# Performance work log

Hardware: AMD Instinct MI355X
Metric: run time of the kernel (lower is better)

The kernel has to match this reference:

```python
import jax, jax.numpy as jnp
import numpy as np

NUM_LAYERS = 3


def setup_inputs() -> dict:
    key = jax.random.key(0)
    k1, k2, k3 = jax.random.split(key, 3)
    B, LT, LC, F = 16, 256, 768, 256
    batch_target = jax.random.normal(k1, (B, LT, F), dtype=jnp.float32)
    batch_claim = jax.random.normal(k2, (B, LC, F), dtype=jnp.float32)
    # adjacency is accepted but mathematically unused (original masked_fill is non-in-place and discarded)
    batch_adj = jax.random.randint(jax.random.fold_in(key, 7), (B, LT + LC, LT + LC), 0, 2, dtype=jnp.int32)
    # per-layer trans_linear weights, nn.Linear(F, F, bias=False): y = x @ W.T, W is [out, in]
    W_trans = jax.random.normal(k3, (NUM_LAYERS, F, F), dtype=jnp.float32) * (1.0 / np.sqrt(F))
    return {"batch_target": batch_target, "batch_claim": batch_claim, "batch_adj": batch_adj, "W_trans": W_trans}


def _gcn_layer(node_rep, W):
    # dot attention: score[b,i,j] = <h_i, h_j>  (symmetric all-pairs dot product)
    # NOTE: original's masked_fill(batch_adj == 0, -1e9) is NOT in-place and its
    # result is discarded, so no masking is applied -- reproduced faithfully here.
    corr = jnp.einsum('bif,bjf->bij', node_rep, node_rep)
    attn = jax.nn.softmax(corr, axis=2)              # softmax over j (dim=2)
    trans = jnp.einsum('blf,gf->blg', node_rep, W)   # trans_linear (bias=False)
    node_out = jax.nn.relu(node_rep + jnp.einsum('bij,bjf->bif', attn, trans))
    return node_out, attn


def reference(batch_target, batch_claim, batch_adj, W_trans):
    target_len = batch_target.shape[1]
    node_rep = jnp.concatenate([batch_target, batch_claim], axis=1)  # [B, L, F]
    all_node_rep, all_corr_score = (), ()
    for i in range(NUM_LAYERS):
        node_rep, corr_score = _gcn_layer(node_rep, W_trans[i])
        all_node_rep = all_node_rep + (node_rep,)
        all_corr_score = all_corr_score + (corr_score,)
        # gcn_dropout: identity in eval mode
    target_rep = node_rep[:, :target_len, :]
    claim_rep = node_rep[:, target_len:, :]
    return (target_rep, claim_rep, all_node_rep, all_corr_score)
```

## Files before the change

### kernel.cpp

```cpp
#include <hip/hip_runtime.h>

typedef _Float16 h16;
typedef _Float16 h16x8 __attribute__((ext_vector_type(8)));
typedef _Float16 h16x4 __attribute__((ext_vector_type(4)));
typedef float    f32x4 __attribute__((ext_vector_type(4)));
typedef float    f32x8 __attribute__((ext_vector_type(8)));

#define NBATCH 16
#define LROWS  1024
#define FDIM   256

#define OFF_TGT 0ull
#define OFF_CLM 1048576ull
#define OFF_NR  4194304ull
#define OFF_AT  16777216ull

__device__ __forceinline__ void split2(float x, h16& h, h16& l) {
    h = (h16)x;
    l = (h16)(x - (float)h);
}

typedef const __attribute__((address_space(1))) void gvoid;
typedef __attribute__((address_space(3))) void lvoid;
__device__ __forceinline__ void gl_lds16(const void* g, void* l) {
    __builtin_amdgcn_global_load_lds((gvoid*)g, (lvoid*)l, 16, 0, 0);
}

__device__ const unsigned char TRI_I[36] = {
    0,0,0,0,0,0,0,0, 1,1,1,1,1,1,1, 2,2,2,2,2,2, 3,3,3,3,3, 4,4,4,4, 5,5,5, 6,6, 7};
__device__ const unsigned char TRI_J[36] = {
    0,1,2,3,4,5,6,7, 1,2,3,4,5,6,7, 2,3,4,5,6,7, 3,4,5,6,7, 4,5,6,7, 5,6,7, 6,7, 7};

__global__ __launch_bounds__(256) void convert_all(const float* __restrict__ tgt,
                                                   const float* __restrict__ clm,
                                                   const float* __restrict__ W,
                                                   h16* __restrict__ xh, h16* __restrict__ xl,
                                                   h16* __restrict__ wh) {
    int bid = blockIdx.x;
    if (bid < 4096) {
        int b, i;
        if (bid < 2048) { b = bid & 7;       i = bid >> 3; }
        else            { b = 8 + (bid & 7); i = (bid - 2048) >> 3; }
        size_t e = ((size_t)b << 18) + (size_t)i * 1024 + (size_t)threadIdx.x * 4;
        int rf = (int)(e & 262143);
        int r  = rf >> 8, f = rf & 255;
        const float* src = (r < 256)
            ? tgt + ((size_t)b << 16) + ((size_t)r << 8) + f
            : clm + (size_t)b * 196608 + ((size_t)(r - 256) << 8) + f;
        f32x4 v = *(const f32x4*)src;
        h16x4 hv, lv;
#pragma unroll
        for (int j = 0; j < 4; ++j) { h16 hh, ll; split2(v[j], hh, ll); hv[j] = hh; lv[j] = ll; }
        *(h16x4*)(xh + e) = hv;
        *(h16x4*)(xl + e) = lv;
    } else {
        size_t e = ((size_t)(bid - 4096) * 256 + threadIdx.x) * 4;
        f32x4 v = *(const f32x4*)(W + e);
        h16x4 hv;
#pragma unroll
        for (int j = 0; j < 4; ++j) hv[j] = (h16)v[j];
        *(h16x4*)(wh + e) = hv;
    }
}

__global__ __launch_bounds__(256, 3) void gemm_ct(
    const h16* __restrict__ Xh, const h16* __restrict__ Xl,
    const h16* __restrict__ Wh,
    h16* __restrict__ Ptil, float2* __restrict__ part,
    h16* __restrict__ Th) {
    int b, u;
    if (blockIdx.x < 416) { b = blockIdx.x & 7;               u = blockIdx.x >> 3; }
    else                  { b = 8 + ((blockIdx.x - 416) & 7); u = (blockIdx.x - 416) >> 3; }
    const bool isCorr = u < 36;
    int it, jt;
    if (isCorr) { it = TRI_I[u]; jt = TRI_J[u]; }
    else        { int v = u - 36; it = v >> 1; jt = v & 1; }
    const bool diag = isCorr && (it == jt);
    const int i0 = it * 128;
    const int j0 = jt * 128;
    const int t  = threadIdx.x;
    const int lane = t & 63, wid = t >> 6;
    const int wr = wid >> 1, wc = wid & 1;

    __shared__ alignas(16) char lds[32768];

    const size_t arow = ((size_t)b * LROWS + i0) * 256;
    const h16* bHp; const h16* bLp; size_t brow;
    if (isCorr) { bHp = Xh; bLp = Xl; brow = ((size_t)b * LROWS + j0) * 256; }
    else        { bHp = Wh; bLp = Xl; brow = (size_t)j0 * 256; }

    const int bOffH = diag ? 0 : 16384;
    const int bOffL = diag ? 8192 : 24576;

    f32x4 acc[4][4];
#pragma unroll
    for (int i = 0; i < 4; ++i)
#pragma unroll
        for (int j = 0; j < 4; ++j) acc[i][j] = (f32x4){0.f, 0.f, 0.f, 0.f};

    const int grow = t >> 2;
    const int gq   = t & 3;

    for (int kt = 0; kt < 8; ++kt) {
        __syncthreads();
#pragma unroll
        for (int p = 0; p < 2; ++p) {
            int r = p * 64 + grow;
            size_t so = (size_t)r * 256 + kt * 32 + ((gq ^ ((r >> 1) & 3)) << 3);
            char* d = lds + p * 4096 + wid * 1024;
            gl_lds16(Xh + arow + so, d);
            gl_lds16(Xl + arow + so, d + 8192);
            if (!diag) {
                gl_lds16(bHp + brow + so, d + 16384);
                if (isCorr) gl_lds16(bLp + brow + so, d + 24576);
            }
        }
        __syncthreads();

        const int kq = lane >> 4;
        const int rA = wr * 64 + (lane & 15);
        const int rB = wc * 64 + (lane & 15);
        h16x8 ah[4], al[4], bh[4], bl[4];
#pragma unroll
        for (int mi = 0; mi < 4; ++mi) {
            int r   = rA + mi * 16;
            int off = r * 64 + ((kq ^ ((r >> 1) & 3)) << 4);
            ah[mi] = *(const h16x8*)(lds + off);
            al[mi] = *(const h16x8*)(lds + 8192 + off);
        }
#pragma unroll
        for (int nj = 0; nj < 4; ++nj) {
            int r   = rB + nj * 16;
            int off = r * 64 + ((kq ^ ((r >> 1) & 3)) << 4);
            bh[nj] = *(const h16x8*)(lds + bOffH + off);
            if (isCorr) bl[nj] = *(const h16x8*)(lds + bOffL + off);
        }
        __builtin_amdgcn_s_setprio(1);
#pragma unroll
        for (int mi = 0; mi < 4; ++mi)
#pragma unroll
            for (int nj = 0; nj < 4; ++nj) {
                acc[mi][nj] = __builtin_amdgcn_mfma_f32_16x16x32_f16(ah[mi], bh[nj], acc[mi][nj], 0, 0, 0);
                acc[mi][nj] = __builtin_amdgcn_mfma_f32_16x16x32_f16(al[mi], bh[nj], acc[mi][nj], 0, 0, 0);
                if (isCorr)
                    acc[mi][nj] = __builtin_amdgcn_mfma_f32_16x16x32_f16(ah[mi], bl[nj], acc[mi][nj], 0, 0, 0);
            }
        __builtin_amdgcn_s_setprio(0);
    }

    const int mBase = i0 + wr * 64;
    const int nBase = j0 + wc * 64;
    if (isCorr) {
        h16* Pb = Ptil + (size_t)b * LROWS * 1024;
        {
            const int chunk = jt * 2 + wc;
#pragma unroll
            for (int mi = 0; mi < 4; ++mi)
#pragma unroll
                for (int rg = 0; rg < 4; ++rg) {
                    float v0 = acc[mi][0][rg], v1 = acc[mi][1][rg];
                    float v2 = acc[mi][2][rg], v3 = acc[mi][3][rg];
                    float mx = fmaxf(fmaxf(v0, v1), fmaxf(v2, v3));
#pragma unroll
                    for (int off = 8; off >= 1; off >>= 1) mx = fmaxf(mx, __shfl_xor(mx, off, 64));
                    float e0 = __expf(v0 - mx), e1 = __expf(v1 - mx);
                    float e2 = __expf(v2 - mx), e3 = __expf(v3 - mx);
                    float s = e0 + e1 + e2 + e3;
#pragma unroll
                    for (int off = 8; off >= 1; off >>= 1) s += __shfl_xor(s, off, 64);
                    int row = mBase + mi * 16 + ((lane >> 4) * 4) + rg;
                    if ((lane & 15) == 0)
                        part[((size_t)b * 1024 + row) * 16 + chunk] = make_float2(mx, s);
                    size_t rb = (size_t)row * 1024 + nBase + (lane & 15);
                    Pb[rb]      = (h16)e0;
                    Pb[rb + 16] = (h16)e1;
                    Pb[rb + 32] = (h16)e2;
                    Pb[rb + 48] = (h16)e3;
                }
        }
        if (it != jt) {
            __syncthreads();
            const int chunk = it * 2 + wr;
            const int cl0 = wc * 64 + (lane & 15);
            const int r40 = wr * 64 + ((lane >> 4) << 2);
#pragma unroll
            for (int nj = 0; nj < 4; ++nj) {
                float mx = -3.0e38f;
#pragma unroll
                for (int mi = 0; mi < 4; ++mi)
#pragma unroll
                    for (int rg = 0; rg < 4; ++rg) mx = fmaxf(mx, acc[mi][nj][rg]);
                mx = fmaxf(mx, __shfl_xor(mx, 16, 64));
                mx = fmaxf(mx, __shfl_xor(mx, 32, 64));
                float s = 0.f;
                h16x4 pt[4];
#pragma unroll
                for (int mi = 0; mi < 4; ++mi)
#pragma unroll
                    for (int rg = 0; rg < 4; ++rg) {
                        float e = __expf(acc[mi][nj][rg] - mx);
                        s += e;
                        pt[mi][rg] = (h16)e;
                    }
                s += __shfl_xor(s, 16, 64);
                s += __shfl_xor(s, 32, 64);
                int n = nBase + nj * 16 + (lane & 15);
                if (lane < 16)
                    part[((size_t)b * 1024 + n) * 16 + chunk] = make_float2(mx, s);
                const int cl = cl0 + nj * 16;
#pragma unroll
                for (int mi = 0; mi < 4; ++mi) {
                    int r4 = r40 + mi * 16;
                    *(h16x4*)(lds + cl * 256 + (((r4 ^ ((cl & 7) << 2))) << 1)) = pt[mi];
                }
            }
            __syncthreads();
#pragma unroll
            for (int i8 = 0; i8 < 8; ++i8) {
                int cl = wid * 32 + i8 * 4 + (lane >> 4);
                int R  = (lane & 15) * 8;
                int k4 = (cl & 7) << 2;
                h16x4 v0 = *(const h16x4*)(lds + cl * 256 + (((R    ) ^ k4) << 1));
                h16x4 v1 = *(const h16x4*)(lds + cl * 256 + (((R + 4) ^ k4) << 1));
                h16x8 vv;
                vv[0] = v0[0]; vv[1] = v0[1]; vv[2] = v0[2]; vv[3] = v0[3];
                vv[4] = v1[0]; vv[5] = v1[1]; vv[6] = v1[2]; vv[7] = v1[3];
                *(h16x8*)(Pb + (size_t)(j0 + cl) * 1024 + i0 + R) = vv;
            }
        }
    } else {
#pragma unroll
        for (int mi = 0; mi < 4; ++mi)
#pragma unroll
            for (int nj = 0; nj < 4; ++nj) {
                int n  = nBase + nj * 16 + (lane & 15);
                int m0 = mBase + mi * 16 + ((lane >> 4) * 4);
                h16x4 hv;
#pragma unroll
                for (int rg = 0; rg < 4; ++rg) hv[rg] = (h16)acc[mi][nj][rg];
                size_t off = ((size_t)b * 256 + n) * 1024 + m0;
                *(h16x4*)(Th + off) = hv;
            }
    }
}

__global__ __launch_bounds__(256, 4) void gemm_pv(
    const h16* __restrict__ Ptil, const float2* __restrict__ part,
    float* __restrict__ At,
    const h16* __restrict__ Th,
    h16* __restrict__ Xh, h16* __restrict__ Xl,
    float* __restrict__ NodeOut, float* __restrict__ OutBase, int last) {
    const int id   = blockIdx.x;
    int b, mt;
    if (id < 256) { b = id & 7;               mt = id >> 3; }
    else          { b = 8 + ((id - 256) & 7); mt = (id - 256) >> 3; }
    const int i0   = mt * 32;
    const int t    = threadIdx.x;
    const int lane = t & 63, wid = t >> 6;
    const int wc   = wid;

    __shared__ alignas(16) char lds[38912];
    float* sc = (float*)(lds + 36864);

    if (t < 32) {
        const float2* pp = part + ((size_t)b * 1024 + i0 + t) * 16;
        float2 v[16];
        float M = -3.0e38f;
#pragma unroll
        for (int c = 0; c < 16; ++c) { v[c] = pp[c]; M = fmaxf(M, v[c].x); }
        float S = 0.f;
#pragma unroll
        for (int c = 0; c < 16; ++c) S += v[c].y * __expf(v[c].x - M);
        float inv = 1.0f / S;
#pragma unroll
        for (int c = 0; c < 16; ++c) sc[t * 16 + c] = __expf(v[c].x - M) * inv;
    }
    __syncthreads();

    const h16* Prow = Ptil + ((size_t)b * LROWS + i0) * 1024;
    float* Arow = At + ((size_t)b * LROWS + i0) * 1024;
    const size_t tbase = (size_t)b * 256 * 1024;

    const int ar = t >> 3;
    const int ac = t & 7;

    f32x4 acc[2][4];
#pragma unroll
    for (int i = 0; i < 2; ++i)
#pragma unroll
        for (int j = 0; j < 4; ++j) acc[i][j] = (f32x4){0.f, 0.f, 0.f, 0.f};

    for (int kt = 0; kt < 16; ++kt) {
        h16x8 pt = *(const h16x8*)(Prow + (size_t)ar * 1024 + kt * 64 + ac * 8);
        float s  = sc[ar * 16 + kt];
        __syncthreads();

#pragma unroll
        for (int itr = 0; itr < 8; ++itr) {
            int g = itr * 32 + ar;
            size_t so = tbase + (size_t)g * 1024 + kt * 64 + ((ac ^ (g & 7)) << 3);
            char* d = lds + 4096 + itr * 4096 + wid * 1024;
            gl_lds16(Th + so, d);
        }

        f32x8 pw;
#pragma unroll
        for (int e = 0; e < 8; ++e) pw[e] = (float)pt[e] * s;
        *(f32x8*)(Arow + (size_t)ar * 1024 + kt * 64 + ac * 8) = pw;
        h16x8 a16;
#pragma unroll
        for (int e = 0; e < 8; ++e) a16[e] = (h16)pw[e];
        *(h16x8*)(lds + ar * 128 + ((ac ^ (ar & 7)) << 4)) = a16;
        __syncthreads();

        const int kq = lane >> 4;
        __builtin_amdgcn_s_setprio(1);
#pragma unroll
        for (int s2 = 0; s2 < 2; ++s2) {
            h16x8 ah[2], bh[4];
#pragma unroll
            for (int mi = 0; mi < 2; ++mi) {
                int r = mi * 16 + (lane & 15);
                ah[mi] = *(const h16x8*)(lds + r * 128 + (((s2 * 4 + kq) ^ (r & 7)) << 4));
            }
#pragma unroll
            for (int nf = 0; nf < 4; ++nf) {
                int g = wc * 64 + nf * 16 + (lane & 15);
                bh[nf] = *(const h16x8*)(lds + 4096 + g * 128 + (((s2 * 4 + kq) ^ (g & 7)) << 4));
            }
#pragma unroll
            for (int mi = 0; mi < 2; ++mi)
#pragma unroll
                for (int nf = 0; nf < 4; ++nf)
                    acc[mi][nf] = __builtin_amdgcn_mfma_f32_16x16x32_f16(ah[mi], bh[nf], acc[mi][nf], 0, 0, 0);
        }
        __builtin_amdgcn_s_setprio(0);
    }

#pragma unroll
    for (int mi = 0; mi < 2; ++mi)
#pragma unroll
        for (int nf = 0; nf < 4; ++nf) {
            int n = wc * 64 + nf * 16 + (lane & 15);
#pragma unroll
            for (int rg = 0; rg < 4; ++rg) {
                int m = i0 + mi * 16 + ((lane >> 4) * 4) + rg;
                size_t off = ((size_t)b * LROWS + m) * FDIM + n;
                float res = (float)Xh[off] + (float)Xl[off];
                float y   = res + acc[mi][nf][rg];
                y = y > 0.f ? y : 0.f;
                NodeOut[off] = y;
                h16 hh, ll; split2(y, hh, ll);
                Xh[off] = hh; Xl[off] = ll;
                if (last) {
                    float* dst = (m < 256)
                        ? OutBase + OFF_TGT + ((size_t)b << 16) + ((size_t)m << 8) + n
                        : OutBase + OFF_CLM + (size_t)b * 196608 + ((size_t)(m - 256) << 8) + n;
                    *dst = y;
                }
            }
        }
}

extern "C" void kernel_launch(void* const* d_in, const int* in_sizes, int n_in,
                              void* d_out, int out_size, void* d_ws, size_t ws_size,
                              hipStream_t stream) {
    (void)in_sizes; (void)n_in; (void)out_size; (void)ws_size;
    const float* tgt = (const float*)d_in[0];
    const float* clm = (const float*)d_in[1];
    const float* W   = (const float*)d_in[3];
    float* out = (float*)d_out;
    char*  ws  = (char*)d_ws;

    h16* xh = (h16*)(ws);
    h16* xl = (h16*)(ws + (8ull << 20));
    h16* th = (h16*)(ws + (16ull << 20));
    h16* wh = (h16*)(ws + (24ull << 20));
    float2* part = (float2*)(ws + (25ull << 20));
    h16* ptil = (h16*)(ws + (27ull << 20));

    convert_all<<<4288, 256, 0, stream>>>(tgt, clm, W, xh, xl, wh);

    for (int L = 0; L < 3; ++L) {
        float* at = out + OFF_AT + (size_t)L * 16777216ull;
        float* nr = out + OFF_NR + (size_t)L * 4194304ull;
        gemm_ct<<<832, 256, 0, stream>>>(xh, xl, wh + (size_t)L * 65536, ptil, part, th);
        gemm_pv<<<512, 256, 0, stream>>>(ptil, part, at, th, xh, xl, nr, out, L == 2);
    }
}
```

Before: 217.2 us.

## Pair gemm_ct tiles per block and halve gemm_pv row tile to 16

gemm_ct now launches 416 blocks, each running two tile work items (u and u+26) in sequence across all 16 batches. This cuts the grid to fit one wave and balances corr and trans tiles per block. gemm_pv moves from 32-row to 16-row output tiles with 1024 blocks, using more parallelism and less LDS per block. In exchange, each block reloads the full Th tile for half as many rows, which doubles Th traffic, and gemm_ct loses block-level parallelism.

Measured after the change: 267.5 us. 1.23x slower.

```diff
diff --git a/kernel.cpp b/kernel.cpp
--- a/kernel.cpp
+++ b/kernel.cpp
@@ -68,179 +68,182 @@
     const h16* __restrict__ Wh,
     h16* __restrict__ Ptil, float2* __restrict__ part,
     h16* __restrict__ Th) {
-    int b, u;
-    if (blockIdx.x < 416) { b = blockIdx.x & 7;               u = blockIdx.x >> 3; }
-    else                  { b = 8 + ((blockIdx.x - 416) & 7); u = (blockIdx.x - 416) >> 3; }
-    const bool isCorr = u < 36;
-    int it, jt;
-    if (isCorr) { it = TRI_I[u]; jt = TRI_J[u]; }
-    else        { int v = u - 36; it = v >> 1; jt = v & 1; }
-    const bool diag = isCorr && (it == jt);
-    const int i0 = it * 128;
-    const int j0 = jt * 128;
+    const int b  = blockIdx.x & 15;
+    const int u0 = blockIdx.x >> 4;
     const int t  = threadIdx.x;
     const int lane = t & 63, wid = t >> 6;
     const int wr = wid >> 1, wc = wid & 1;
 
     __shared__ alignas(16) char lds[32768];
 
-    const size_t arow = ((size_t)b * LROWS + i0) * 256;
-    const h16* bHp; const h16* bLp; size_t brow;
-    if (isCorr) { bHp = Xh; bLp = Xl; brow = ((size_t)b * LROWS + j0) * 256; }
-    else        { bHp = Wh; bLp = Xl; brow = (size_t)j0 * 256; }
-
-    const int bOffH = diag ? 0 : 16384;
-    const int bOffL = diag ? 8192 : 24576;
-
-    f32x4 acc[4][4];
-#pragma unroll
-    for (int i = 0; i < 4; ++i)
-#pragma unroll
-        for (int j = 0; j < 4; ++j) acc[i][j] = (f32x4){0.f, 0.f, 0.f, 0.f};
-
-    const int grow = t >> 2;
-    const int gq   = t & 3;
-
-    for (int kt = 0; kt < 8; ++kt) {
-        __syncthreads();
-#pragma unroll
-        for (int p = 0; p < 2; ++p) {
-            int r = p * 64 + grow;
-            size_t so = (size_t)r * 256 + kt * 32 + ((gq ^ ((r >> 1) & 3)) << 3);
-            char* d = lds + p * 4096 + wid * 1024;
-            gl_lds16(Xh + arow + so, d);
-            gl_lds16(Xl + arow + so, d + 8192);
-            if (!diag) {
-                gl_lds16(bHp + brow + so, d + 16384);
-                if (isCorr) gl_lds16(bLp + brow + so, d + 24576);
-            }
-        }
-        __syncthreads();
-
-        const int kq = lane >> 4;
-        const int rA = wr * 64 + (lane & 15);
-        const int rB = wc * 64 + (lane & 15);
-        h16x8 ah[4], al[4], bh[4], bl[4];
-#pragma unroll
-        for (int mi = 0; mi < 4; ++mi) {
-            int r   = rA + mi * 16;
-            int off = r * 64 + ((kq ^ ((r >> 1) & 3)) << 4);
-            ah[mi] = *(const h16x8*)(lds + off);
-            al[mi] = *(const h16x8*)(lds + 8192 + off);
-        }
-#pragma unroll
-        for (int nj = 0; nj < 4; ++nj) {
-            int r   = rB + nj * 16;
-            int off = r * 64 + ((kq ^ ((r >> 1) & 3)) << 4);
-            bh[nj] = *(const h16x8*)(lds + bOffH + off);
-            if (isCorr) bl[nj] = *(const h16x8*)(lds + bOffL + off);
-        }
-        __builtin_amdgcn_s_setprio(1);
-#pragma unroll
-        for (int mi = 0; mi < 4; ++mi)
+    for (int half = 0; half < 2; ++half) {
+        const int u = u0 + half * 26;
+        const bool isCorr = u < 36;
+        int it, jt;
+        if (isCorr) { it = TRI_I[u]; jt = TRI_J[u]; }
+        else        { int v = u - 36; it = v >> 1; jt = v & 1; }
+        const bool diag = isCorr && (it == jt);
+        const int i0 = it * 128;
+        const int j0 = jt * 128;
+
+        const size_t arow = ((size_t)b * LROWS + i0) * 256;
+        const h16* bHp; const h16* bLp; size_t brow;
+        if (isCorr) { bHp = Xh; bLp = Xl; brow = ((size_t)b * LROWS + j0) * 256; }
+        else        { bHp = Wh; bLp = Xl; brow = (size_t)j0 * 256; }
+
+        const int bOffH = diag ? 0 : 16384;
+        const int bOffL = diag ? 8192 : 24576;
+
+        f32x4 acc[4][4];
+#pragma unroll
+        for (int i = 0; i < 4; ++i)
+#pragma unroll
+            for (int j = 0; j < 4; ++j) acc[i][j] = (f32x4){0.f, 0.f, 0.f, 0.f};
+
+        const int grow = t >> 2;
+        const int gq   = t & 3;
+
+        for (int kt = 0; kt < 8; ++kt) {
+            __syncthreads();
+#pragma unroll
+            for (int p = 0; p < 2; ++p) {
+                int r = p * 64 + grow;
+                size_t so = (size_t)r * 256 + kt * 32 + ((gq ^ ((r >> 1) & 3)) << 3);
+                char* d = lds + p * 4096 + wid * 1024;
+                gl_lds16(Xh + arow + so, d);
+                gl_lds16(Xl + arow + so, d + 8192);
+                if (!diag) {
+                    gl_lds16(bHp + brow + so, d + 16384);
+                    if (isCorr) gl_lds16(bLp + brow + so, d + 24576);
+                }
+            }
+            __syncthreads();
+
+            const int kq = lane >> 4;
+            const int rA = wr * 64 + (lane & 15);
+            const int rB = wc * 64 + (lane & 15);
+            h16x8 ah[4], al[4], bh[4], bl[4];
+#pragma unroll
+            for (int mi = 0; mi < 4; ++mi) {
+                int r   = rA + mi * 16;
+                int off = r * 64 + ((kq ^ ((r >> 1) & 3)) << 4);
+                ah[mi] = *(const h16x8*)(lds + off);
+                al[mi] = *(const h16x8*)(lds + 8192 + off);
+            }
 #pragma unroll
             for (int nj = 0; nj < 4; ++nj) {
-                acc[mi][nj] = __builtin_amdgcn_mfma_f32_16x16x32_f16(ah[mi], bh[nj], acc[mi][nj], 0, 0, 0);
-                acc[mi][nj] = __builtin_amdgcn_mfma_f32_16x16x32_f16(al[mi], bh[nj], acc[mi][nj], 0, 0, 0);
-                if (isCorr)
-                    acc[mi][nj] = __builtin_amdgcn_mfma_f32_16x16x32_f16(ah[mi], bl[nj], acc[mi][nj], 0, 0, 0);
-            }
-        __builtin_amdgcn_s_setprio(0);
-    }
-
-    const int mBase = i0 + wr * 64;
-    const int nBase = j0 + wc * 64;
-    if (isCorr) {
-        h16* Pb = Ptil + (size_t)b * LROWS * 1024;
-        {
-            const int chunk = jt * 2 + wc;
+                int r   = rB + nj * 16;
+                int off = r * 64 + ((kq ^ ((r >> 1) & 3)) << 4);
+                bh[nj] = *(const h16x8*)(lds + bOffH + off);
+                if (isCorr) bl[nj] = *(const h16x8*)(lds + bOffL + off);
+            }
+            __builtin_amdgcn_s_setprio(1);
 #pragma unroll
             for (int mi = 0; mi < 4; ++mi)
 #pragma unroll
-                for (int rg = 0; rg < 4; ++rg) {
-                    float v0 = acc[mi][0][rg], v1 = acc[mi][1][rg];
-                    float v2 = acc[mi][2][rg], v3 = acc[mi][3][rg];
-                    float mx = fmaxf(fmaxf(v0, v1), fmaxf(v2, v3));
-#pragma unroll
-                    for (int off = 8; off >= 1; off >>= 1) mx = fmaxf(mx, __shfl_xor(mx, off, 64));
-                    float e0 = __expf(v0 - mx), e1 = __expf(v1 - mx);
-                    float e2 = __expf(v2 - mx), e3 = __expf(v3 - mx);
-                    float s = e0 + e1 + e2 + e3;
-#pragma unroll
-                    for (int off = 8; off >= 1; off >>= 1) s += __shfl_xor(s, off, 64);
-                    int row = mBase + mi * 16 + ((lane >> 4) * 4) + rg;
-                    if ((lane & 15) == 0)
-                        part[((size_t)b * 1024 + row) * 16 + chunk] = make_float2(mx, s);
-                    size_t rb = (size_t)row * 1024 + nBase + (lane & 15);
-                    Pb[rb]      = (h16)e0;
-                    Pb[rb + 16] = (h16)e1;
-                    Pb[rb + 32] = (h16)e2;
-                    Pb[rb + 48] = (h16)e3;
-                }
-        }
-        if (it != jt) {
-            __syncthreads();
-            const int chunk = it * 2 + wr;
-            const int cl0 = wc * 64 + (lane & 15);
-            const int r40 = wr * 64 + ((lane >> 4) << 2);
-#pragma unroll
-            for (int nj = 0; nj < 4; ++nj) {
-                float mx = -3.0e38f;
+                for (int nj = 0; nj < 4; ++nj) {
+                    acc[mi][nj] = __builtin_amdgcn_mfma_f32_16x16x32_f16(ah[mi], bh[nj], acc[mi][nj], 0, 0, 0);
+                    acc[mi][nj] = __builtin_amdgcn_mfma_f32_16x16x32_f16(al[mi], bh[nj], acc[mi][nj], 0, 0, 0);
+                    if (isCorr)
+                        acc[mi][nj] = __builtin_amdgcn_mfma_f32_16x16x32_f16(ah[mi], bl[nj], acc[mi][nj], 0, 0, 0);
+                }
+            __builtin_amdgcn_s_setprio(0);
+        }
+
+        const int mBase = i0 + wr * 64;
+        const int nBase = j0 + wc * 64;
+        if (isCorr) {
+            h16* Pb = Ptil + (size_t)b * LROWS * 1024;
+            {
+                const int chunk = jt * 2 + wc;
 #pragma unroll
                 for (int mi = 0; mi < 4; ++mi)
 #pragma unroll
-                    for (int rg = 0; rg < 4; ++rg) mx = fmaxf(mx, acc[mi][nj][rg]);
-                mx = fmaxf(mx, __shfl_xor(mx, 16, 64));
-                mx = fmaxf(mx, __shfl_xor(mx, 32, 64));
-                float s = 0.f;
-                h16x4 pt[4];
-#pragma unroll
-                for (int mi = 0; mi < 4; ++mi)
-#pragma unroll
                     for (int rg = 0; rg < 4; ++rg) {
-                        float e = __expf(acc[mi][nj][rg] - mx);
-                        s += e;
-                        pt[mi][rg] = (h16)e;
+                        float v0 = acc[mi][0][rg], v1 = acc[mi][1][rg];
+                        float v2 = acc[mi][2][rg], v3 = acc[mi][3][rg];
+                        float mx = fmaxf(fmaxf(v0, v1), fmaxf(v2, v3));
+#pragma unroll
+                        for (int off = 8; off >= 1; off >>= 1) mx = fmaxf(mx, __shfl_xor(mx, off, 64));
+                        float e0 = __expf(v0 - mx), e1 = __expf(v1 - mx);
+                        float e2 = __expf(v2 - mx), e3 = __expf(v3 - mx);
+                        float s = e0 + e1 + e2 + e3;
+#pragma unroll
+                        for (int off = 8; off >= 1; off >>= 1) s += __shfl_xor(s, off, 64);
+                        int row = mBase + mi * 16 + ((lane >> 4) * 4) + rg;
+                        if ((lane & 15) == 0)
+                            part[((size_t)b * 1024 + row) * 16 + chunk] = make_float2(mx, s);
+                        size_t rb = (size_t)row * 1024 + nBase + (lane & 15);
+                        Pb[rb]      = (h16)e0;
+                        Pb[rb + 16] = (h16)e1;
+                        Pb[rb + 32] = (h16)e2;
+                        Pb[rb + 48] = (h16)e3;
                     }
-                s += __shfl_xor(s, 16, 64);
-                s += __shfl_xor(s, 32, 64);
-                int n = nBase + nj * 16 + (lane & 15);
-                if (lane < 16)
-                    part[((size_t)b * 1024 + n) * 16 + chunk] = make_float2(mx, s);
-                const int cl = cl0 + nj * 16;
-#pragma unroll
-                for (int mi = 0; mi < 4; ++mi) {
-                    int r4 = r40 + mi * 16;
-                    *(h16x4*)(lds + cl * 256 + (((r4 ^ ((cl & 7) << 2))) << 1)) = pt[mi];
-                }
-            }
-            __syncthreads();
-#pragma unroll
-            for (int i8 = 0; i8 < 8; ++i8) {
-                int cl = wid * 32 + i8 * 4 + (lane >> 4);
-                int R  = (lane & 15) * 8;
-                int k4 = (cl & 7) << 2;
-                h16x4 v0 = *(const h16x4*)(lds + cl * 256 + (((R    ) ^ k4) << 1));
-                h16x4 v1 = *(const h16x4*)(lds + cl * 256 + (((R + 4) ^ k4) << 1));
-                h16x8 vv;
-                vv[0] = v0[0]; vv[1] = v0[1]; vv[2] = v0[2]; vv[3] = v0[3];
-                vv[4] = v1[0]; vv[5] = v1[1]; vv[6] = v1[2]; vv[7] = v1[3];
-                *(h16x8*)(Pb + (size_t)(j0 + cl) * 1024 + i0 + R) = vv;
-            }
-        }
-    } else {
-#pragma unroll
-        for (int mi = 0; mi < 4; ++mi)
-#pragma unroll
-            for (int nj = 0; nj < 4; ++nj) {
-                int n  = nBase + nj * 16 + (lane & 15);
-                int m0 = mBase + mi * 16 + ((lane >> 4) * 4);
-                h16x4 hv;
-#pragma unroll
-                for (int rg = 0; rg < 4; ++rg) hv[rg] = (h16)acc[mi][nj][rg];
-                size_t off = ((size_t)b * 256 + n) * 1024 + m0;
-                *(h16x4*)(Th + off) = hv;
-            }
+            }
+            if (it != jt) {
+                __syncthreads();
+                const int chunk = it * 2 + wr;
+                const int cl0 = wc * 64 + (lane & 15);
+                const int r40 = wr * 64 + ((lane >> 4) << 2);
+#pragma unroll
+                for (int nj = 0; nj < 4; ++nj) {
+                    float mx = -3.0e38f;
+#pragma unroll
+                    for (int mi = 0; mi < 4; ++mi)
+#pragma unroll
+                        for (int rg = 0; rg < 4; ++rg) mx = fmaxf(mx, acc[mi][nj][rg]);
+                    mx = fmaxf(mx, __shfl_xor(mx, 16, 64));
+                    mx = fmaxf(mx, __shfl_xor(mx, 32, 64));
+                    float s = 0.f;
+                    h16x4 pt[4];
+#pragma unroll
+                    for (int mi = 0; mi < 4; ++mi)
+#pragma unroll
+                        for (int rg = 0; rg < 4; ++rg) {
+                            float e = __expf(acc[mi][nj][rg] - mx);
+                            s += e;
+                            pt[mi][rg] = (h16)e;
+                        }
+                    s += __shfl_xor(s, 16, 64);
+                    s += __shfl_xor(s, 32, 64);
+                    int n = nBase + nj * 16 + (lane & 15);
+                    if (lane < 16)
+                        part[((size_t)b * 1024 + n) * 16 + chunk] = make_float2(mx, s);
+                    const int cl = cl0 + nj * 16;
+#pragma unroll
+                    for (int mi = 0; mi < 4; ++mi) {
+                        int r4 = r40 + mi * 16;
+                        *(h16x4*)(lds + cl * 256 + (((r4 ^ ((cl & 7) << 2))) << 1)) = pt[mi];
+                    }
+                }
+                __syncthreads();
+#pragma unroll
+                for (int i8 = 0; i8 < 8; ++i8) {
+                    int cl = wid * 32 + i8 * 4 + (lane >> 4);
+                    int R  = (lane & 15) * 8;
+                    int k4 = (cl & 7) << 2;
+                    h16x4 v0 = *(const h16x4*)(lds + cl * 256 + (((R    ) ^ k4) << 1));
+                    h16x4 v1 = *(const h16x4*)(lds + cl * 256 + (((R + 4) ^ k4) << 1));
+                    h16x8 vv;
+                    vv[0] = v0[0]; vv[1] = v0[1]; vv[2] = v0[2]; vv[3] = v0[3];
+                    vv[4] = v1[0]; vv[5] = v1[1]; vv[6] = v1[2]; vv[7] = v1[3];
+                    *(h16x8*)(Pb + (size_t)(j0 + cl) * 1024 + i0 + R) = vv;
+                }
+            }
+        } else {
+#pragma unroll
+            for (int mi = 0; mi < 4; ++mi)
+#pragma unroll
+                for (int nj = 0; nj < 4; ++nj) {
+                    int n  = nBase + nj * 16 + (lane & 15);
+                    int m0 = mBase + mi * 16 + ((lane >> 4) * 4);
+                    h16x4 hv;
+#pragma unroll
+                    for (int rg = 0; rg < 4; ++rg) hv[rg] = (h16)acc[mi][nj][rg];
+                    size_t off = ((size_t)b * 256 + n) * 1024 + m0;
+                    *(h16x4*)(Th + off) = hv;
+                }
+        }
     }
 }
 
@@ -251,18 +254,17 @@
     h16* __restrict__ Xh, h16* __restrict__ Xl,
     float* __restrict__ NodeOut, float* __restrict__ OutBase, int last) {
     const int id   = blockIdx.x;
-    int b, mt;
-    if (id < 256) { b = id & 7;               mt = id >> 3; }
-    else          { b = 8 + ((id - 256) & 7); mt = (id - 256) >> 3; }
-    const int i0   = mt * 32;
+    const int b    = (id & 7) | (((id >> 3) & 1) << 3);
+    const int mt   = id >> 4;
+    const int i0   = mt * 16;
     const int t    = threadIdx.x;
     const int lane = t & 63, wid = t >> 6;
     const int wc   = wid;
 
-    __shared__ alignas(16) char lds[38912];
-    float* sc = (float*)(lds + 36864);
-
-    if (t < 32) {
+    __shared__ alignas(16) char lds[35840];
+    float* sc = (float*)(lds + 34816);
+
+    if (t < 16) {
         const float2* pp = part + ((size_t)b * 1024 + i0 + t) * 16;
         float2 v[16];
         float M = -3.0e38f;
@@ -281,85 +283,78 @@
     float* Arow = At + ((size_t)b * LROWS + i0) * 1024;
     const size_t tbase = (size_t)b * 256 * 1024;
 
-    const int ar = t >> 3;
-    const int ac = t & 7;
-
-    f32x4 acc[2][4];
-#pragma unroll
-    for (int i = 0; i < 2; ++i)
-#pragma unroll
-        for (int j = 0; j < 4; ++j) acc[i][j] = (f32x4){0.f, 0.f, 0.f, 0.f};
+    const int ar = t >> 4;
+    const int ac = t & 15;
+    const int bgr = t >> 3;
+    const int bq  = t & 7;
+
+    f32x4 acc[4];
+#pragma unroll
+    for (int i = 0; i < 4; ++i) acc[i] = (f32x4){0.f, 0.f, 0.f, 0.f};
 
     for (int kt = 0; kt < 16; ++kt) {
-        h16x8 pt = *(const h16x8*)(Prow + (size_t)ar * 1024 + kt * 64 + ac * 8);
+        h16x4 pt = *(const h16x4*)(Prow + (size_t)ar * 1024 + kt * 64 + ac * 4);
         float s  = sc[ar * 16 + kt];
         __syncthreads();
 
 #pragma unroll
         for (int itr = 0; itr < 8; ++itr) {
-            int g = itr * 32 + ar;
-            size_t so = tbase + (size_t)g * 1024 + kt * 64 + ((ac ^ (g & 7)) << 3);
-            char* d = lds + 4096 + itr * 4096 + wid * 1024;
+            int g = itr * 32 + bgr;
+            size_t so = tbase + (size_t)g * 1024 + kt * 64 + ((bq ^ (g & 7)) << 3);
+            char* d = lds + 2048 + itr * 4096 + wid * 1024;
             gl_lds16(Th + so, d);
         }
 
-        f32x8 pw;
-#pragma unroll
-        for (int e = 0; e < 8; ++e) pw[e] = (float)pt[e] * s;
-        *(f32x8*)(Arow + (size_t)ar * 1024 + kt * 64 + ac * 8) = pw;
-        h16x8 a16;
-#pragma unroll
-        for (int e = 0; e < 8; ++e) a16[e] = (h16)pw[e];
-        *(h16x8*)(lds + ar * 128 + ((ac ^ (ar & 7)) << 4)) = a16;
+        f32x4 pw;
+#pragma unroll
+        for (int e = 0; e < 4; ++e) pw[e] = (float)pt[e] * s;
+        *(f32x4*)(Arow + (size_t)ar * 1024 + kt * 64 + ac * 4) = pw;
+        h16x4 a16;
+#pragma unroll
+        for (int e = 0; e < 4; ++e) a16[e] = (h16)pw[e];
+        {
+            int c = ac >> 1, hb = (ac & 1) * 8;
+            *(h16x4*)(lds + ar * 128 + ((c ^ (ar & 7)) << 4) + hb) = a16;
+        }
         __syncthreads();
 
         const int kq = lane >> 4;
         __builtin_amdgcn_s_setprio(1);
 #pragma unroll
         for (int s2 = 0; s2 < 2; ++s2) {
-            h16x8 ah[2], bh[4];
-#pragma unroll
-            for (int mi = 0; mi < 2; ++mi) {
-                int r = mi * 16 + (lane & 15);
-                ah[mi] = *(const h16x8*)(lds + r * 128 + (((s2 * 4 + kq) ^ (r & 7)) << 4));
-            }
+            int r = lane & 15;
+            h16x8 ah = *(const h16x8*)(lds + r * 128 + (((s2 * 4 + kq) ^ (r & 7)) << 4));
 #pragma unroll
             for (int nf = 0; nf < 4; ++nf) {
                 int g = wc * 64 + nf * 16 + (lane & 15);
-                bh[nf] = *(const h16x8*)(lds + 4096 + g * 128 + (((s2 * 4 + kq) ^ (g & 7)) << 4));
-            }
-#pragma unroll
-            for (int mi = 0; mi < 2; ++mi)
-#pragma unroll
-                for (int nf = 0; nf < 4; ++nf)
-                    acc[mi][nf] = __builtin_amdgcn_mfma_f32_16x16x32_f16(ah[mi], bh[nf], acc[mi][nf], 0, 0, 0);
+                h16x8 bh = *(const h16x8*)(lds + 2048 + g * 128 + (((s2 * 4 + kq) ^ (g & 7)) << 4));
+                acc[nf] = __builtin_amdgcn_mfma_f32_16x16x32_f16(ah, bh, acc[nf], 0, 0, 0);
+            }
         }
         __builtin_amdgcn_s_setprio(0);
     }
 
 #pragma unroll
-    for (int mi = 0; mi < 2; ++mi)
-#pragma unroll
-        for (int nf = 0; nf < 4; ++nf) {
-            int n = wc * 64 + nf * 16 + (lane & 15);
-#pragma unroll
-            for (int rg = 0; rg < 4; ++rg) {
-                int m = i0 + mi * 16 + ((lane >> 4) * 4) + rg;
-                size_t off = ((size_t)b * LROWS + m) * FDIM + n;
-                float res = (float)Xh[off] + (float)Xl[off];
-                float y   = res + acc[mi][nf][rg];
-                y = y > 0.f ? y : 0.f;
-                NodeOut[off] = y;
-                h16 hh, ll; split2(y, hh, ll);
-                Xh[off] = hh; Xl[off] = ll;
-                if (last) {
-                    float* dst = (m < 256)
-                        ? OutBase + OFF_TGT + ((size_t)b << 16) + ((size_t)m << 8) + n
-                        : OutBase + OFF_CLM + (size_t)b * 196608 + ((size_t)(m - 256) << 8) + n;
-                    *dst = y;
-                }
-            }
-        }
+    for (int nf = 0; nf < 4; ++nf) {
+        int n = wc * 64 + nf * 16 + (lane & 15);
+#pragma unroll
+        for (int rg = 0; rg < 4; ++rg) {
+            int m = i0 + ((lane >> 4) * 4) + rg;
+            size_t off = ((size_t)b * LROWS + m) * FDIM + n;
+            float res = (float)Xh[off] + (float)Xl[off];
+            float y   = res + acc[nf][rg];
+            y = y > 0.f ? y : 0.f;
+            NodeOut[off] = y;
+            h16 hh, ll; split2(y, hh, ll);
+            Xh[off] = hh; Xl[off] = ll;
+            if (last) {
+                float* dst = (m < 256)
+                    ? OutBase + OFF_TGT + ((size_t)b << 16) + ((size_t)m << 8) + n
+                    : OutBase + OFF_CLM + (size_t)b * 196608 + ((size_t)(m - 256) << 8) + n;
+                *dst = y;
+            }
+        }
+    }
 }
 
 extern "C" void kernel_launch(void* const* d_in, const int* in_sizes, int n_in,
@@ -384,7 +379,7 @@
     for (int L = 0; L < 3; ++L) {
         float* at = out + OFF_AT + (size_t)L * 16777216ull;
         float* nr = out + OFF_NR + (size_t)L * 4194304ull;
-        gemm_ct<<<832, 256, 0, stream>>>(xh, xl, wh + (size_t)L * 65536, ptil, part, th);
-        gemm_pv<<<512, 256, 0, stream>>>(ptil, part, at, th, xh, xl, nr, out, L == 2);
-    }
-}
+        gemm_ct<<<416, 256, 0, stream>>>(xh, xl, wh + (size_t)L * 65536, ptil, part, th);
+        gemm_pv<<<1024, 256, 0, stream>>>(ptil, part, at, th, xh, xl, nr, out, L == 2);
+    }
+}
```
